# Performance work log

Hardware: AMD Instinct MI355X
Metric: run time of the kernel (lower is better)

The kernel has to match this reference:

```python
import jax, jax.numpy as jnp
import numpy as np

S, B, L = 64, 32, 64
VS, VT = 32000, 32000
D_EMB, H_ENC, H_DEC = 300, 512, 1024


def _lstm_cell(x, h, c, w_ih, w_hh, b):
    # PyTorch gate order: i, f, g, o
    g = x @ w_ih.T + h @ w_hh.T + b
    i, f, gg, o = jnp.split(g, 4, axis=1)
    c2 = jax.nn.sigmoid(f) * c + jax.nn.sigmoid(i) * jnp.tanh(gg)
    h2 = jax.nn.sigmoid(o) * jnp.tanh(c2)
    return h2, c2


def _lstm_dir(emb, w_ih, w_hh, b, reverse):
    h0 = jnp.zeros((emb.shape[1], H_ENC), emb.dtype)
    def step(carry, x):
        h, c = carry
        h, c = _lstm_cell(x, h, c, w_ih, w_hh, b)
        return (h, c), h
    (hT, cT), ys = jax.lax.scan(step, (h0, h0), emb, reverse=reverse)
    return ys, hT, cT


def setup_inputs() -> dict:
    key = jax.random.key(0)
    ks = jax.random.split(key, 20)
    r = lambda k, shape: (jax.random.normal(k, shape, jnp.float32) * 0.02)
    inp = {
        "eemb": r(ks[0], (VS, D_EMB)),
        "enc_w_ih_f": r(ks[1], (4 * H_ENC, D_EMB)),
        "enc_w_hh_f": r(ks[2], (4 * H_ENC, H_ENC)),
        "enc_b_f": r(ks[3], (4 * H_ENC,)),  # = b_ih + b_hh (summed, identical math)
        "enc_w_ih_b": r(ks[4], (4 * H_ENC, D_EMB)),
        "enc_w_hh_b": r(ks[5], (4 * H_ENC, H_ENC)),
        "enc_b_b": r(ks[6], (4 * H_ENC,)),
        "attn_wi": r(ks[7], (H_DEC, H_DEC)),
        "attn_wo": r(ks[8], (H_DEC, 2 * H_DEC)),
        "dec_w_ih": r(ks[9], (4 * H_DEC, H_DEC + D_EMB)),
        "dec_w_hh": r(ks[10], (4 * H_DEC, H_DEC)),
        "dec_b": r(ks[11], (4 * H_DEC,)),
        "demb": r(ks[12], (VT, D_EMB)),
        "gen_w": r(ks[13], (VT, H_DEC)),
        "gen_b": r(ks[14], (VT,)),
        "input_src_batch": jax.random.randint(ks[15], (S, B), 0, VS),
        "input_trg_batch": jax.random.randint(ks[16], (L, B), 0, VT),
    }
    return inp


def reference(eemb, enc_w_ih_f, enc_w_hh_f, enc_b_f, enc_w_ih_b, enc_w_hh_b,
              enc_b_b, attn_wi, attn_wo, dec_w_ih, dec_w_hh, dec_b, demb,
              gen_w, gen_b, input_src_batch, input_trg_batch):
    emb = eemb[input_src_batch]  # [S,B,300]
    out_f, hf, cf = _lstm_dir(emb, enc_w_ih_f, enc_w_hh_f, enc_b_f, False)
    out_b, hb, cb = _lstm_dir(emb, enc_w_ih_b, enc_w_hh_b, enc_b_b, True)
    enc_out = jnp.concatenate([out_f, out_b], axis=2)  # [S,B,1024]
    bsz = emb.shape[1]
    # permute(1,2,0).view(B,1024): interleave fwd/bwd features
    hidden = jnp.stack([hf, hb], 0).transpose(1, 2, 0).reshape(bsz, H_DEC)
    context = jnp.stack([cf, cb], 0).transpose(1, 2, 0).reshape(bsz, H_DEC)

    trg_emb = demb[input_trg_batch[:-1]]  # [L-1,B,300]

    def dec_step(carry, e):
        h, c = carry
        semi = h @ attn_wi.T  # [B,1024]
        scores = jax.nn.softmax(jnp.sum(enc_out * semi[None], axis=2), axis=0)  # [S,B]
        s_tilde = jnp.sum(scores[:, :, None] * enc_out, axis=0)  # [B,1024]
        c_t = jnp.tanh(jnp.concatenate([s_tilde, h], axis=1) @ attn_wo.T)
        x = jnp.concatenate([c_t, e], axis=1)  # [B,1324]
        h, c = _lstm_cell(x, h, c, dec_w_ih, dec_w_hh, dec_b)
        out = jax.nn.log_softmax(h @ gen_w.T + gen_b, axis=1)  # [B,VT]
        return (h, c), out

    _, ys = jax.lax.scan(dec_step, (hidden, context), trg_emb)  # [L-1,B,VT]
    output = jnp.concatenate([jnp.zeros((1,) + ys.shape[1:], ys.dtype), ys], axis=0)
    return output
```

## Files before the change

kernel.cpp:

```cpp
#include <hip/hip_runtime.h>

typedef __attribute__((ext_vector_type(8))) short short8;
typedef __attribute__((ext_vector_type(4))) float f32x4;
typedef unsigned short u16;
typedef unsigned int u32;

static __device__ __forceinline__ float sigf(float x){ return 1.0f/(1.0f+__expf(-x)); }
static __device__ __forceinline__ float ftanh(float x){
    float e = __expf(2.0f*x);
    return 1.0f - 2.0f/(e + 1.0f);
}

static __device__ __forceinline__ u16 f2b(float f){
    u32 u = __float_as_uint(f);
    u += 0x7FFFu + ((u>>16)&1u);
    return (u16)(u>>16);
}
static __device__ __forceinline__ float us2f(u16 s){ return __uint_as_float(((u32)s)<<16); }
static __device__ __forceinline__ float b2f_lo(u32 u){ return __uint_as_float(u<<16); }
static __device__ __forceinline__ float b2f_hi(u32 u){ return __uint_as_float(u & 0xffff0000u); }

static __device__ __forceinline__ void st_wt_u16(u16* p, u16 v) {
    asm volatile("global_store_short %0, %1, off sc1" :: "v"(p), "v"((u32)v) : "memory");
}
static __device__ __forceinline__ void st_wt_u32(u32* p, u32 v) {
    asm volatile("global_store_dword %0, %1, off sc1" :: "v"(p), "v"(v) : "memory");
}
static __device__ __forceinline__ u32 ld_cv(const u32* p){
    u32 v;
    asm volatile("global_load_dword %0, %1, off sc0 sc1\ns_waitcnt vmcnt(0)"
                 : "=v"(v) : "v"(p) : "memory");
    return v;
}

static __device__ __forceinline__ void hot_spin() {
    float x = 1.0f;
#pragma unroll
    for (int i = 0; i < 16; ++i) x = __builtin_fmaf(x, 1.0000001f, 1.0e-7f);
    asm volatile("" :: "v"(x));
}

static __device__ __forceinline__ void wait_publish(const u32* base, int n, u32 tgt, u32* rel) {
    if ((int)threadIdx.x < n) {
        const u32* p = base + (size_t)threadIdx.x*32;
        while (ld_cv(p) < tgt) hot_spin();
    }
    __syncthreads();
    if (threadIdx.x == 0) st_wt_u32(rel, tgt);
}
static __device__ __forceinline__ void wait_rel(const u32* rel, u32 tgt) {
    if (threadIdx.x == 0) {
        while (ld_cv(rel) < tgt) hot_spin();
    }
    __syncthreads();
}


__global__ __launch_bounds__(256) void k_zero(float* __restrict__ p, long n) {
    for (long i = (long)blockIdx.x*256 + threadIdx.x; i < n; i += (long)gridDim.x*256) p[i] = 0.0f;
}

__global__ __launch_bounds__(256) void k_wenc2(const float* __restrict__ whhf,
                                               const float* __restrict__ whhb,
                                               u16* __restrict__ dst) {
    long i = (long)blockIdx.x*256 + threadIdx.x;
    int half = (int)(i >> 20);
    int ii = (int)(i & 1048575);
    int n = ii >> 9, k = ii & 511;
    int j = n >> 2, q = n & 3;
    const float* w = half ? whhb : whhf;
    dst[i] = f2b(w[(size_t)(q*512 + j)*512 + k]);
}

__global__ __launch_bounds__(256) void k_xw(const float* __restrict__ table,
                                            const int* __restrict__ idx,
                                            const float* __restrict__ W,
                                            int wstride, int koff,
                                            const float* __restrict__ bias,
                                            u16* __restrict__ outU, int N,
                                            int jmask, int jshift) {
    __shared__ float Xs[32][300];
    int m0 = blockIdx.y * 32;
    int j0 = blockIdx.x * 64;
    for (int i = threadIdx.x; i < 32*300; i += 256) {
        int r = i/300, c = i - r*300;
        Xs[r][c] = table[(size_t)idx[m0+r]*300 + c];
    }
    __syncthreads();
    int tx = threadIdx.x & 63, ty = threadIdx.x >> 6;
    int jj = j0 + tx;
    const float* wr = W + (size_t)jj*wstride + koff;
    float acc[8] = {0,0,0,0,0,0,0,0};
    for (int k = 0; k < 300; ++k) {
        float w = wr[k];
#pragma unroll
        for (int mi = 0; mi < 8; ++mi) acc[mi] += Xs[ty*8+mi][k] * w;
    }
    float bv = bias[jj];
    int col = ((jj & jmask) << 2) | (jj >> jshift);
#pragma unroll
    for (int mi = 0; mi < 8; ++mi)
        outU[(size_t)(m0 + ty*8 + mi)*N + col] = f2b(acc[mi] + bv);
}

__global__ __launch_bounds__(512, 1) void k_enc(
    const u16* __restrict__ Xf, const u16* __restrict__ Xb,
    const u16* __restrict__ WencB,
    u16* __restrict__ encBX, float* __restrict__ cfin,
    u32* __restrict__ sentE, u32* __restrict__ relE,
    const float* __restrict__ awi, const float* __restrict__ awo,
    const float* __restrict__ dwih, const float* __restrict__ dwhh,
    const float* __restrict__ genw,
    u16* __restrict__ awiTB, u16* __restrict__ awoB,
    u16* __restrict__ WdecB, u16* __restrict__ genw_b)
{
    __shared__ float SH[2304];
    const int tid = threadIdx.x;
    const int bid = blockIdx.x;

    if (bid >= 64) {
        long wid = (long)(bid-64)*512 + tid;
        {
            const float4* s4 = (const float4*)genw;
            ushort4* d4 = (ushort4*)genw_b;
            for (long i = wid; i < 8192000L; i += 98304L) {
                float4 v = s4[i]; ushort4 u;
                u.x=f2b(v.x); u.y=f2b(v.y); u.z=f2b(v.z); u.w=f2b(v.w);
                d4[i]=u;
            }
        }
        for (long i = wid; i < 8388608L; i += 98304L) {
            int n=(int)(i>>11), k=(int)(i&2047);
            int j=n>>2, q=n&3;
            float v=(k<1024)? dwih[(size_t)(q*1024+j)*1324+k]
                            : dwhh[(size_t)(q*1024+j)*1024+(k-1024)];
            WdecB[i]=f2b(v);
        }
        for (long i = wid; i < 1048576L; i += 98304L) {
            int kcol=(int)(i>>10), n=(int)(i&1023);
            awiTB[i]=f2b(awi[(size_t)n*1024+kcol]);
        }
        {
            const float4* s4=(const float4*)awo;
            ushort4* d4=(ushort4*)awoB;
            for (long i = wid; i < 524288L; i += 98304L) {
                float4 v=s4[i]; ushort4 u;
                u.x=f2b(v.x); u.y=f2b(v.y); u.z=f2b(v.z); u.w=f2b(v.w);
                d4[i]=u;
            }
        }
        return;
    }

    const int wv = tid >> 6, lane = tid & 63;
    const int gwave = bid*8 + wv;
    const int lr = lane & 15, lk8 = (lane >> 4)*8;
    const int b_l = lane & 15, jjq = lane >> 4;
    const int g0 = bid & 48;
    u32* relg = relE + (size_t)(g0 >> 4)*32;

    const int dir = gwave >> 8;
    const int mt = (gwave >> 7) & 1;
    const int nt = gwave & 127;
    const int m0 = mt*16, n0 = nt*16;
    const u16* Bw = WencB + (size_t)dir*1048576 + (size_t)(n0+lr)*512 + lk8;
    const u16* Xd = dir ? Xb : Xf;
    float* T = SH + wv*272;
    const int bb = m0 + b_l;
    const int j = nt*4 + jjq;

    short8 bw[16];
#pragma unroll
    for (int i = 0; i < 16; ++i) bw[i] = *(const short8*)(Bw + i*32);

    float creg = 0.f;
    for (int t = 0; t < 64; ++t) {
        if (t > 0) {
            if (bid == g0) wait_publish(sentE + (size_t)g0*32, 16, (u32)t, relg);
            else           wait_rel(relg, (u32)t);
        }
        const int rslot = (t==0) ? 0 : (dir ? (65-t) : t);
        const u16* Ah = encBX + (size_t)rslot*32768 + (size_t)(m0+lr)*1024 + dir*512 + lk8;
        short8 av[16];
#pragma unroll
        for (int i = 0; i < 16; ++i) av[i] = *(const short8*)(Ah + i*32);
        f32x4 acc = {0.f,0.f,0.f,0.f};
#pragma unroll
        for (int i = 0; i < 16; ++i)
            acc = __builtin_amdgcn_mfma_f32_16x16x32_bf16(av[i], bw[i], acc, 0, 0, 0);
        {
            const int rb = (lane>>4)*4;
#pragma unroll
            for (int r = 0; r < 4; ++r) T[(rb+r)*17 + (lane&15)] = acc[r];
        }
        __builtin_amdgcn_sched_barrier(0);
        const int s = dir ? (63-t) : t;
        ushort4 xr = *(const ushort4*)(Xd + (size_t)(s*32+bb)*2048 + n0 + jjq*4);
        float gi = T[b_l*17 + jjq*4 + 0] + us2f(xr.x);
        float gf = T[b_l*17 + jjq*4 + 1] + us2f(xr.y);
        float gg = T[b_l*17 + jjq*4 + 2] + us2f(xr.z);
        float go = T[b_l*17 + jjq*4 + 3] + us2f(xr.w);
        float c2 = sigf(gf)*creg + sigf(gi)*ftanh(gg);
        float h2 = sigf(go)*ftanh(c2);
        creg = c2;
        st_wt_u16(encBX + (size_t)(s+1)*32768 + (size_t)bb*1024 + dir*512 + j, f2b(h2));
        __syncthreads();
        if (tid == 0) st_wt_u32(sentE + (size_t)bid*32, (u32)(t+1));
    }
    cfin[dir*16384 + bb*512 + j] = creg;
}

__global__ __launch_bounds__(256) void k_mid(const u16* __restrict__ encBX,
                                             const u16* __restrict__ awiTB,
                                             const u16* __restrict__ awoB,
                                             u16* __restrict__ encPB,
                                             u16* __restrict__ EOAb,
                                             u16* __restrict__ Hd) {
    if (blockIdx.x < 128) {
        int gt = blockIdx.x*256 + threadIdx.x;
        int b = gt >> 10, jj2 = gt & 1023;
        int d = jj2 & 1, k = jj2 >> 1;
        Hd[(size_t)b*1024 + jj2] = encBX[(size_t)(d ? 1 : 64)*32768 + (size_t)b*1024 + d*512 + k];
        Hd[(size_t)64*32768 + gt] = 0;
    }
    const int wv = threadIdx.x >> 6, lane = threadIdx.x & 63;
    const int lr = lane & 15, lk8 = (lane >> 4)*8;
    const u16* Abase = encBX + 32768;
#pragma unroll
    for (int ii = 0; ii < 4; ++ii) {
        int id = (blockIdx.x*4 + wv)*4 + ii;
        int eoa = id >> 13;
        int id2 = id & 8191;
        int mt2 = id2 >> 6, nt2 = id2 & 63;
        int m0 = mt2*16, n0 = nt2*16;
        const u16* Ar = Abase + (size_t)(m0+lr)*1024 + lk8;
        const u16* Br = eoa ? (awoB + (size_t)(n0+lr)*2048 + lk8)
                            : (awiTB + (size_t)(n0+lr)*1024 + lk8);
        f32x4 acc = {0.f,0.f,0.f,0.f};
#pragma unroll 8
        for (int i = 0; i < 32; ++i) {
            short8 av = *(const short8*)(Ar + i*32);
            short8 bv = *(const short8*)(Br + i*32);
            acc = __builtin_amdgcn_mfma_f32_16x16x32_bf16(av, bv, acc, 0, 0, 0);
        }
        int col = n0 + (lane&15);
        int rb = m0 + (lane>>4)*4;
#pragma unroll
        for (int r = 0; r < 4; ++r) {
            int row = rb + r;
            if (eoa) {
                int b = row & 31, s = row >> 5;
                EOAb[((size_t)b*64 + s)*1024 + col] = f2b(acc[r]);
            } else {
                encPB[(size_t)row*1024 + col] = f2b(acc[r]);
            }
        }
    }
}

__global__ __launch_bounds__(512, 1) void k_dec(
    const u16* __restrict__ Xe,
    const u16* __restrict__ awoB, const u16* __restrict__ WdecB,
    const u16* __restrict__ encPB, const u16* __restrict__ EOAb,
    u16* __restrict__ Hd, u16* __restrict__ PEOb, u16* __restrict__ hAb,
    const float* __restrict__ cfin,
    const u16* __restrict__ genw_b, const float* __restrict__ genb, float* __restrict__ out,
    u32* __restrict__ sentA, u32* __restrict__ sentH,
    u32* __restrict__ relA, u32* __restrict__ relH)
{
    __shared__ float SH[5184];
    __shared__ u32 CT[16512];
    const int tid = threadIdx.x;
    const int bid = blockIdx.x;
    const int wv = tid >> 6, lane = tid & 63;
    const int lr = lane & 15, lk8 = (lane >> 4)*8;
    const int b_l = lane & 15, jjq = lane >> 4;

    if (bid >= 128) {
        const int gw = (bid - 128)*8 + wv;
        const u16* A = Hd + 32768;
        for (int c = 0; c < 8; ++c) {
            u32 need = (c == 7) ? 63u : (u32)(8*c + 8);
            wait_rel(relH, need);
            int tile = gw;
            if (tile < 1000) {
                int m0 = c*256 + (tile & 1)*128;
                int n0 = (tile >> 1)*64;
                f32x4 acc[8][4] = {};
                for (int k0 = 0; k0 < 1024; k0 += 32) {
                    short8 bfr[4];
#pragma unroll
                    for (int ni = 0; ni < 4; ++ni)
                        bfr[ni] = *(const short8*)(genw_b + (size_t)(n0 + ni*16 + lr)*1024 + k0 + lk8);
#pragma unroll
                    for (int mi = 0; mi < 8; ++mi) {
                        short8 a = *(const short8*)(A + (size_t)(m0 + mi*16 + lr)*1024 + k0 + lk8);
#pragma unroll
                        for (int ni = 0; ni < 4; ++ni)
                            acc[mi][ni] = __builtin_amdgcn_mfma_f32_16x16x32_bf16(a, bfr[ni], acc[mi][ni], 0, 0, 0);
                    }
                }
                int dcol = lane & 15;
                int drow = (lane >> 4)*4;
#pragma unroll
                for (int mi = 0; mi < 8; ++mi) {
                    int mbase = m0 + mi*16 + drow;
#pragma unroll
                    for (int ni = 0; ni < 4; ++ni) {
                        int n = n0 + ni*16 + dcol;
                        float bv = genb[n];
                        f32x4 v = acc[mi][ni];
#pragma unroll
                        for (int r = 0; r < 4; ++r) {
                            int m = mbase + r;
                            if (m < 2016) out[(size_t)(m + 32)*32000 + n] = v[r] + bv;
                        }
                    }
                }
            }
        }
        return;
    }

    const int ntB = wv & 1, kqB = wv >> 1;
    const int jdB = bid*8 + ntB*4 + jjq;
    float cdec0 = 0.f, cdec1 = 0.f;
    if (wv < 2) {
        cdec0 = cfin[(jdB&1)*16384 + (b_l)*512 + (jdB>>1)];
        cdec1 = cfin[(jdB&1)*16384 + (16+b_l)*512 + (jdB>>1)];
    }

    short8 wp[16];
#pragma unroll
    for (int i = 0; i < 16; ++i)
        wp[i] = *(const short8*)(WdecB + (size_t)(bid*32 + ntB*16 + lr)*2048 + kqB*512 + lk8 + i*32);

    const bool isHA = (bid >= 32 && bid < 96);
    const int nth = bid - 32;
    const int mth = wv & 1, kqh = wv >> 1;
    short8 wh[8];
    if (isHA) {
#pragma unroll
        for (int i = 0; i < 8; ++i)
            wh[i] = *(const short8*)(awoB + (size_t)(nth*16+lr)*2048 + 1024 + kqh*256 + lk8 + i*32);
    }

    for (int t = 0; t < 63; ++t) {
        if (t > 0 && bid == 97) wait_publish(sentH, 128, (u32)t, relH);
        if (bid < 96) {
            if (t > 0) wait_rel(relH, (u32)t);
            if (bid < 32) {
                const int b = bid;
                float* hsh = SH; float* red = SH + 1024; float* sc = SH + 1536;
                {
                    u32 u = ((const u32*)Hd)[(size_t)t*16384 + b*512 + tid];
                    hsh[2*tid]   = b2f_lo(u);
                    hsh[2*tid+1] = b2f_hi(u);
                }
                __syncthreads();
                {
                    int s = tid >> 3, p = tid & 7;
                    const uint4* ep = (const uint4*)(encPB + (size_t)(s*32+b)*1024 + p*128);
                    const float* hk = hsh + p*128;
                    float a0=0,a1=0,a2=0,a3=0;
#pragma unroll 4
                    for (int q8 = 0; q8 < 16; ++q8) {
                        uint4 u = ep[q8];
                        a0 += b2f_lo(u.x)*hk[q8*8+0] + b2f_hi(u.x)*hk[q8*8+1];
                        a1 += b2f_lo(u.y)*hk[q8*8+2] + b2f_hi(u.y)*hk[q8*8+3];
                        a2 += b2f_lo(u.z)*hk[q8*8+4] + b2f_hi(u.z)*hk[q8*8+5];
                        a3 += b2f_lo(u.w)*hk[q8*8+6] + b2f_hi(u.w)*hk[q8*8+7];
                    }
                    red[tid] = (a0+a1)+(a2+a3);
                }
                __syncthreads();
                if (tid < 64) {
                    float v = 0;
#pragma unroll
                    for (int pp = 0; pp < 8; ++pp) v += red[tid*8+pp];
                    float m = v;
                    for (int off = 32; off; off >>= 1) m = fmaxf(m, __shfl_xor(m, off));
                    float e = __expf(v - m);
                    float ss = e;
                    for (int off = 32; off; off >>= 1) ss += __shfl_xor(ss, off);
                    sc[tid] = e / ss;
                }
                __syncthreads();
                {
                    const u32* eo = (const u32*)EOAb + (size_t)b*32768 + tid;
                    float p0 = 0, p1 = 0;
#pragma unroll 8
                    for (int s = 0; s < 64; ++s) {
                        u32 u = eo[(size_t)s*512];
                        float w = sc[s];
                        p0 += w*b2f_lo(u); p1 += w*b2f_hi(u);
                    }
                    u32 pk = (u32)f2b(p0) | ((u32)f2b(p1) << 16);
                    st_wt_u32((u32*)PEOb + (size_t)t*16384 + b*512 + tid, pk);
                }
            } else {
                const u16* Ah = Hd + (size_t)t*32768 + (size_t)(mth*16+lr)*1024 + kqh*256 + lk8;
                short8 av[8];
#pragma unroll
                for (int i = 0; i < 8; ++i) av[i] = *(const short8*)(Ah + i*32);
                f32x4 acc = {0.f,0.f,0.f,0.f};
#pragma unroll
                for (int i = 0; i < 8; ++i)
                    acc = __builtin_amdgcn_mfma_f32_16x16x32_bf16(av[i], wh[i], acc, 0, 0, 0);
#pragma unroll
                for (int r = 0; r < 4; ++r) SH[wv*256 + lane*4 + r] = acc[r];
                __syncthreads();
                if (wv < 2) {
#pragma unroll
                    for (int r = 0; r < 4; ++r) {
                        float sum = SH[(wv+0)*256 + lane*4 + r] + SH[(wv+2)*256 + lane*4 + r]
                                  + SH[(wv+4)*256 + lane*4 + r] + SH[(wv+6)*256 + lane*4 + r];
                        int m = wv*16 + (lane>>4)*4 + r;
                        st_wt_u16(hAb + (size_t)t*32768 + (size_t)m*1024 + nth*16 + (lane&15),
                                  f2b(sum));
                    }
                }
            }
            __syncthreads();
            if (tid == 0) st_wt_u32(sentA + (size_t)bid*32, (u32)(t+1));
        }

        if (bid == 96) wait_publish(sentA, 96, (u32)(t+1), relA);
        else           wait_rel(relA, (u32)(t+1));
        {
            const u32* pe = (const u32*)PEOb + (size_t)t*16384;
            const u32* ha = (const u32*)hAb + (size_t)t*16384;
#pragma unroll
            for (int ii = 0; ii < 32; ++ii) {
                int idx = tid + ii*512;
                u32 up = pe[idx], uh = ha[idx];
                float c0 = ftanh(b2f_lo(up) + b2f_lo(uh));
                float c1 = ftanh(b2f_hi(up) + b2f_hi(uh));
                int b = idx >> 9, nu = idx & 511;
                CT[b*516 + nu] = (u32)f2b(c0) | ((u32)f2b(c1) << 16);
            }
            __syncthreads();

            f32x4 a0 = {0.f,0.f,0.f,0.f}, a1 = {0.f,0.f,0.f,0.f};
            if (kqB < 2) {
                const u32* c0p = CT + (lr)*516 + kqB*256 + (lk8 >> 1);
                const u32* c1p = CT + (16+lr)*516 + kqB*256 + (lk8 >> 1);
#pragma unroll
                for (int i = 0; i < 16; ++i) {
                    short8 v0 = *(const short8*)(c0p + i*16);
                    short8 v1 = *(const short8*)(c1p + i*16);
                    a0 = __builtin_amdgcn_mfma_f32_16x16x32_bf16(v0, wp[i], a0, 0, 0, 0);
                    a1 = __builtin_amdgcn_mfma_f32_16x16x32_bf16(v1, wp[i], a1, 0, 0, 0);
                }
            } else {
                const u16* h0p = Hd + (size_t)t*32768 + (size_t)(lr)*1024 + (kqB-2)*512 + lk8;
                const u16* h1p = Hd + (size_t)t*32768 + (size_t)(16+lr)*1024 + (kqB-2)*512 + lk8;
#pragma unroll
                for (int i = 0; i < 16; ++i) {
                    short8 v0 = *(const short8*)(h0p + i*32);
                    short8 v1 = *(const short8*)(h1p + i*32);
                    a0 = __builtin_amdgcn_mfma_f32_16x16x32_bf16(v0, wp[i], a0, 0, 0, 0);
                    a1 = __builtin_amdgcn_mfma_f32_16x16x32_bf16(v1, wp[i], a1, 0, 0, 0);
                }
            }
#pragma unroll
            for (int r = 0; r < 4; ++r) {
                SH[wv*512 + lane*4 + r] = a0[r];
                SH[wv*512 + 256 + lane*4 + r] = a1[r];
            }
            __syncthreads();
            if (wv < 2) {
                const int nt = wv;
                float* T0 = SH + 4096 + (wv*2+0)*272;
                float* T1 = SH + 4096 + (wv*2+1)*272;
#pragma unroll
                for (int r = 0; r < 4; ++r) {
                    float s0 = SH[(nt+0)*512 + lane*4 + r] + SH[(nt+2)*512 + lane*4 + r]
                             + SH[(nt+4)*512 + lane*4 + r] + SH[(nt+6)*512 + lane*4 + r];
                    float s1 = SH[(nt+0)*512 + 256 + lane*4 + r] + SH[(nt+2)*512 + 256 + lane*4 + r]
                             + SH[(nt+4)*512 + 256 + lane*4 + r] + SH[(nt+6)*512 + 256 + lane*4 + r];
                    int rr = ((lane>>4)*4 + r)*17 + (lane&15);
                    T0[rr] = s0;
                    T1[rr] = s1;
                }
                __builtin_amdgcn_sched_barrier(0);
                {
                    ushort4 xr = *(const ushort4*)(Xe + (size_t)(t*32 + b_l)*4096 + jdB*4);
                    float gi = T0[b_l*17 + jjq*4 + 0] + us2f(xr.x);
                    float gf = T0[b_l*17 + jjq*4 + 1] + us2f(xr.y);
                    float gg = T0[b_l*17 + jjq*4 + 2] + us2f(xr.z);
                    float go = T0[b_l*17 + jjq*4 + 3] + us2f(xr.w);
                    float c2 = sigf(gf)*cdec0 + sigf(gi)*ftanh(gg);
                    float h2 = sigf(go)*ftanh(c2);
                    cdec0 = c2;
                    st_wt_u16(Hd + (size_t)(t+1)*32768 + (size_t)b_l*1024 + jdB, f2b(h2));
                }
                {
                    ushort4 xr = *(const ushort4*)(Xe + (size_t)(t*32 + 16 + b_l)*4096 + jdB*4);
                    float gi = T1[b_l*17 + jjq*4 + 0] + us2f(xr.x);
                    float gf = T1[b_l*17 + jjq*4 + 1] + us2f(xr.y);
                    float gg = T1[b_l*17 + jjq*4 + 2] + us2f(xr.z);
                    float go = T1[b_l*17 + jjq*4 + 3] + us2f(xr.w);
                    float c2 = sigf(gf)*cdec1 + sigf(gi)*ftanh(gg);
                    float h2 = sigf(go)*ftanh(c2);
                    cdec1 = c2;
                    st_wt_u16(Hd + (size_t)(t+1)*32768 + (size_t)(16+b_l)*1024 + jdB, f2b(h2));
                }
            }
            __syncthreads();
            if (tid == 0) st_wt_u32(sentH + (size_t)bid*32, (u32)(t+1));
        }
    }
    if (bid == 97) wait_publish(sentH, 128, 63u, relH);
}

__global__ __launch_bounds__(256) void k_lsm(float* __restrict__ out) {
    long row = 32 + blockIdx.x;
    float* p = out + row*32000L;
    float4* p4 = (float4*)p;
    int tid = threadIdx.x;
    __shared__ float sm[4];
    __shared__ float ss[4];
    float m = -1e30f;
    for (int i = tid; i < 8000; i += 256) {
        float4 v = p4[i];
        m = fmaxf(m, fmaxf(fmaxf(v.x, v.y), fmaxf(v.z, v.w)));
    }
    for (int off = 32; off; off >>= 1) m = fmaxf(m, __shfl_xor(m, off));
    if ((tid & 63) == 0) sm[tid >> 6] = m;
    __syncthreads();
    m = fmaxf(fmaxf(sm[0], sm[1]), fmaxf(sm[2], sm[3]));
    float s = 0;
    for (int i = tid; i < 8000; i += 256) {
        float4 v = p4[i];
        s += __expf(v.x - m) + __expf(v.y - m) + __expf(v.z - m) + __expf(v.w - m);
    }
    for (int off = 32; off; off >>= 1) s += __shfl_xor(s, off);
    if ((tid & 63) == 0) ss[tid >> 6] = s;
    __syncthreads();
    s = ss[0] + ss[1] + ss[2] + ss[3];
    float lse = m + __logf(s);
    for (int i = tid; i < 8000; i += 256) {
        float4 v = p4[i];
        v.x -= lse; v.y -= lse; v.z -= lse; v.w -= lse;
        p4[i] = v;
    }
}


extern "C" void kernel_launch(void* const* d_in, const int* in_sizes, int n_in,
                              void* d_out, int out_size, void* d_ws, size_t ws_size,
                              hipStream_t stream) {
    const float* eemb  = (const float*)d_in[0];
    const float* ewihf = (const float*)d_in[1];
    const float* ewhhf = (const float*)d_in[2];
    const float* ebf   = (const float*)d_in[3];
    const float* ewihb = (const float*)d_in[4];
    const float* ewhhb = (const float*)d_in[5];
    const float* ebb   = (const float*)d_in[6];
    const float* awi   = (const float*)d_in[7];
    const float* awo   = (const float*)d_in[8];
    const float* dwih  = (const float*)d_in[9];
    const float* dwhh  = (const float*)d_in[10];
    const float* db    = (const float*)d_in[11];
    const float* demb  = (const float*)d_in[12];
    const float* genw  = (const float*)d_in[13];
    const float* genb  = (const float*)d_in[14];
    const int* srci    = (const int*)d_in[15];
    const int* trgi    = (const int*)d_in[16];
    float* out = (float*)d_out;

    float* F = (float*)d_ws;
    u32* S       = (u32*)F;
    u32* sentE   = S;
    u32* sentA   = S + 2048;
    u32* sentH   = S + 5120;
    u32* relE    = S + 13312;
    u32* relA    = S + 13440;
    u32* relH    = S + 13472;
    float* cfin  = F + 16384;
    u16*   U     = (u16*)(F + 49152);

    u16* Xf_    = U;
    u16* Xb_    = U + 4194304u;
    u16* Xe_    = U + 8388608u;
    u16* WencB  = U + 16646144u;
    u16* awiTB  = U + 18743296u;
    u16* awoB   = U + 19791872u;
    u16* WdecB  = U + 21889024u;
    u16* genw_b = U + 30277632u;
    u16* encBX  = U + 63045632u;
    u16* Hd     = U + 65175552u;
    u16* PEOb   = U + 67305472u;
    u16* hAb    = U + 69369856u;
    u16* encPB  = U + 71434240u;
    u16* EOAb   = U + 73531392u;

    k_zero<<<64, 256, 0, stream>>>(F, 16384);
    k_zero<<<64, 256, 0, stream>>>((float*)encBX, 16384);
    k_zero<<<2048, 256, 0, stream>>>(out, 1024000L);

    k_xw<<<dim3(32, 64), 256, 0, stream>>>(eemb, srci, ewihf, 300, 0, ebf, Xf_, 2048, 511, 9);
    k_xw<<<dim3(32, 64), 256, 0, stream>>>(eemb, srci, ewihb, 300, 0, ebb, Xb_, 2048, 511, 9);
    k_xw<<<dim3(64, 63), 256, 0, stream>>>(demb, trgi, dwih, 1324, 1024, db, Xe_, 4096, 1023, 10);

    k_wenc2<<<8192, 256, 0, stream>>>(ewhhf, ewhhb, WencB);

    k_enc<<<256, 512, 0, stream>>>(Xf_, Xb_, WencB, encBX, cfin, sentE, relE,
                                   awi, awo, dwih, dwhh, genw,
                                   awiTB, awoB, WdecB, genw_b);
    k_mid<<<1024, 256, 0, stream>>>(encBX, awiTB, awoB, encPB, EOAb, Hd);

    k_dec<<<256, 512, 0, stream>>>(Xe_, awoB, WdecB, encPB, EOAb,
                                   Hd, PEOb, hAb, cfin,
                                   genw_b, genb, out,
                                   sentA, sentH, relA, relH);

    k_lsm<<<2016, 256, 0, stream>>>(out);
}
```

Measured before the change: 2.480 ms.

## Halve encoder LSTM blocks with two N-tiles per wave and fold zeroing into weight prep

The encoder recurrence now uses 32 blocks instead of 64, with each wave computing two 16-column tiles that share one A-operand load per step. Each synchronisation group shrinks from 16 to 8 blocks, which cuts barrier fan-in per timestep. The freed blocks are handed to the weight-conversion work, so 224 blocks now do it. The two separate zeroing launches are folded into the weight-prep kernel. The cost is twice the MFMA work and register pressure per wave on the serial critical path.

Result: slower. 2.570 ms (+3.6%).

```diff
diff --git a/kernel.cpp b/kernel.cpp
--- a/kernel.cpp
+++ b/kernel.cpp
@@ -62,7 +62,14 @@
 
 __global__ __launch_bounds__(256) void k_wenc2(const float* __restrict__ whhf,
                                                const float* __restrict__ whhb,
-                                               u16* __restrict__ dst) {
+                                               u16* __restrict__ dst,
+                                               float* __restrict__ sentF,
+                                               float* __restrict__ encBX0) {
+    if (blockIdx.x < 64) {
+        sentF[blockIdx.x*256 + threadIdx.x] = 0.0f;
+    } else if (blockIdx.x < 128) {
+        encBX0[(blockIdx.x-64)*256 + threadIdx.x] = 0.0f;
+    }
     long i = (long)blockIdx.x*256 + threadIdx.x;
     int half = (int)(i >> 20);
     int ii = (int)(i & 1048575);
@@ -114,36 +121,36 @@
     u16* __restrict__ awiTB, u16* __restrict__ awoB,
     u16* __restrict__ WdecB, u16* __restrict__ genw_b)
 {
-    __shared__ float SH[2304];
+    __shared__ float SH[4224];
     const int tid = threadIdx.x;
     const int bid = blockIdx.x;
 
-    if (bid >= 64) {
-        long wid = (long)(bid-64)*512 + tid;
+    if (bid >= 32) {
+        long wid = (long)(bid-32)*512 + tid;
         {
             const float4* s4 = (const float4*)genw;
             ushort4* d4 = (ushort4*)genw_b;
-            for (long i = wid; i < 8192000L; i += 98304L) {
+            for (long i = wid; i < 8192000L; i += 114688L) {
                 float4 v = s4[i]; ushort4 u;
                 u.x=f2b(v.x); u.y=f2b(v.y); u.z=f2b(v.z); u.w=f2b(v.w);
                 d4[i]=u;
             }
         }
-        for (long i = wid; i < 8388608L; i += 98304L) {
+        for (long i = wid; i < 8388608L; i += 114688L) {
             int n=(int)(i>>11), k=(int)(i&2047);
             int j=n>>2, q=n&3;
             float v=(k<1024)? dwih[(size_t)(q*1024+j)*1324+k]
                             : dwhh[(size_t)(q*1024+j)*1024+(k-1024)];
             WdecB[i]=f2b(v);
         }
-        for (long i = wid; i < 1048576L; i += 98304L) {
+        for (long i = wid; i < 1048576L; i += 114688L) {
             int kcol=(int)(i>>10), n=(int)(i&1023);
             awiTB[i]=f2b(awi[(size_t)n*1024+kcol]);
         }
         {
             const float4* s4=(const float4*)awo;
             ushort4* d4=(ushort4*)awoB;
-            for (long i = wid; i < 524288L; i += 98304L) {
+            for (long i = wid; i < 524288L; i += 114688L) {
                 float4 v=s4[i]; ushort4 u;
                 u.x=f2b(v.x); u.y=f2b(v.y); u.z=f2b(v.z); u.w=f2b(v.w);
                 d4[i]=u;
@@ -153,61 +160,74 @@
     }
 
     const int wv = tid >> 6, lane = tid & 63;
-    const int gwave = bid*8 + wv;
     const int lr = lane & 15, lk8 = (lane >> 4)*8;
     const int b_l = lane & 15, jjq = lane >> 4;
-    const int g0 = bid & 48;
-    u32* relg = relE + (size_t)(g0 >> 4)*32;
-
-    const int dir = gwave >> 8;
-    const int mt = (gwave >> 7) & 1;
-    const int nt = gwave & 127;
-    const int m0 = mt*16, n0 = nt*16;
-    const u16* Bw = WencB + (size_t)dir*1048576 + (size_t)(n0+lr)*512 + lk8;
+
+    const int dir = bid >> 4;
+    const int mt  = (bid >> 3) & 1;
+    const int g0  = bid & 24;
+    u32* relg = relE + (size_t)(g0 >> 3)*32;
+
+    const int n0 = ((bid & 7)*8 + wv)*32;
+    const int m0 = mt*16;
     const u16* Xd = dir ? Xb : Xf;
-    float* T = SH + wv*272;
+    float* T = SH + wv*528;
     const int bb = m0 + b_l;
-    const int j = nt*4 + jjq;
-
-    short8 bw[16];
-#pragma unroll
-    for (int i = 0; i < 16; ++i) bw[i] = *(const short8*)(Bw + i*32);
-
-    float creg = 0.f;
+    const int jb = n0 >> 2;
+
+    short8 bw0[16], bw1[16];
+    {
+        const u16* B0 = WencB + (size_t)dir*1048576 + (size_t)(n0+lr)*512 + lk8;
+        const u16* B1 = WencB + (size_t)dir*1048576 + (size_t)(n0+16+lr)*512 + lk8;
+#pragma unroll
+        for (int i = 0; i < 16; ++i) { bw0[i] = *(const short8*)(B0 + i*32);
+                                       bw1[i] = *(const short8*)(B1 + i*32); }
+    }
+
+    float creg[2] = {0.f, 0.f};
     for (int t = 0; t < 64; ++t) {
         if (t > 0) {
-            if (bid == g0) wait_publish(sentE + (size_t)g0*32, 16, (u32)t, relg);
+            if (bid == g0) wait_publish(sentE + (size_t)g0*32, 8, (u32)t, relg);
             else           wait_rel(relg, (u32)t);
         }
         const int rslot = (t==0) ? 0 : (dir ? (65-t) : t);
         const u16* Ah = encBX + (size_t)rslot*32768 + (size_t)(m0+lr)*1024 + dir*512 + lk8;
-        short8 av[16];
-#pragma unroll
-        for (int i = 0; i < 16; ++i) av[i] = *(const short8*)(Ah + i*32);
-        f32x4 acc = {0.f,0.f,0.f,0.f};
-#pragma unroll
-        for (int i = 0; i < 16; ++i)
-            acc = __builtin_amdgcn_mfma_f32_16x16x32_bf16(av[i], bw[i], acc, 0, 0, 0);
+        f32x4 acc0 = {0.f,0.f,0.f,0.f}, acc1 = {0.f,0.f,0.f,0.f};
+#pragma unroll
+        for (int i = 0; i < 16; ++i) {
+            short8 av = *(const short8*)(Ah + i*32);
+            acc0 = __builtin_amdgcn_mfma_f32_16x16x32_bf16(av, bw0[i], acc0, 0, 0, 0);
+            acc1 = __builtin_amdgcn_mfma_f32_16x16x32_bf16(av, bw1[i], acc1, 0, 0, 0);
+        }
         {
             const int rb = (lane>>4)*4;
 #pragma unroll
-            for (int r = 0; r < 4; ++r) T[(rb+r)*17 + (lane&15)] = acc[r];
+            for (int r = 0; r < 4; ++r) {
+                T[(rb+r)*33 + (lane&15)]      = acc0[r];
+                T[(rb+r)*33 + 16 + (lane&15)] = acc1[r];
+            }
         }
         __builtin_amdgcn_sched_barrier(0);
         const int s = dir ? (63-t) : t;
-        ushort4 xr = *(const ushort4*)(Xd + (size_t)(s*32+bb)*2048 + n0 + jjq*4);
-        float gi = T[b_l*17 + jjq*4 + 0] + us2f(xr.x);
-        float gf = T[b_l*17 + jjq*4 + 1] + us2f(xr.y);
-        float gg = T[b_l*17 + jjq*4 + 2] + us2f(xr.z);
-        float go = T[b_l*17 + jjq*4 + 3] + us2f(xr.w);
-        float c2 = sigf(gf)*creg + sigf(gi)*ftanh(gg);
-        float h2 = sigf(go)*ftanh(c2);
-        creg = c2;
-        st_wt_u16(encBX + (size_t)(s+1)*32768 + (size_t)bb*1024 + dir*512 + j, f2b(h2));
+#pragma unroll
+        for (int jj2 = 0; jj2 < 2; ++jj2) {
+            const int j = jb + jj2*4 + jjq;
+            ushort4 xr = *(const ushort4*)(Xd + (size_t)(s*32+bb)*2048 + j*4);
+            float gi = T[b_l*33 + jj2*16 + jjq*4 + 0] + us2f(xr.x);
+            float gf = T[b_l*33 + jj2*16 + jjq*4 + 1] + us2f(xr.y);
+            float gg = T[b_l*33 + jj2*16 + jjq*4 + 2] + us2f(xr.z);
+            float go = T[b_l*33 + jj2*16 + jjq*4 + 3] + us2f(xr.w);
+            float c2 = sigf(gf)*creg[jj2] + sigf(gi)*ftanh(gg);
+            float h2 = sigf(go)*ftanh(c2);
+            creg[jj2] = c2;
+            st_wt_u16(encBX + (size_t)(s+1)*32768 + (size_t)bb*1024 + dir*512 + j, f2b(h2));
+        }
         __syncthreads();
         if (tid == 0) st_wt_u32(sentE + (size_t)bid*32, (u32)(t+1));
     }
-    cfin[dir*16384 + bb*512 + j] = creg;
+#pragma unroll
+    for (int jj2 = 0; jj2 < 2; ++jj2)
+        cfin[dir*16384 + bb*512 + (jb + jj2*4 + jjq)] = creg[jj2];
 }
 
 __global__ __launch_bounds__(256) void k_mid(const u16* __restrict__ encBX,
@@ -596,15 +616,13 @@
     u16* encPB  = U + 71434240u;
     u16* EOAb   = U + 73531392u;
 
-    k_zero<<<64, 256, 0, stream>>>(F, 16384);
-    k_zero<<<64, 256, 0, stream>>>((float*)encBX, 16384);
     k_zero<<<2048, 256, 0, stream>>>(out, 1024000L);
 
     k_xw<<<dim3(32, 64), 256, 0, stream>>>(eemb, srci, ewihf, 300, 0, ebf, Xf_, 2048, 511, 9);
     k_xw<<<dim3(32, 64), 256, 0, stream>>>(eemb, srci, ewihb, 300, 0, ebb, Xb_, 2048, 511, 9);
     k_xw<<<dim3(64, 63), 256, 0, stream>>>(demb, trgi, dwih, 1324, 1024, db, Xe_, 4096, 1023, 10);
 
-    k_wenc2<<<8192, 256, 0, stream>>>(ewhhf, ewhhb, WencB);
+    k_wenc2<<<8192, 256, 0, stream>>>(ewhhf, ewhhb, WencB, F, (float*)encBX);
 
     k_enc<<<256, 512, 0, stream>>>(Xf_, Xb_, WencB, encBX, cfin, sentE, relE,
                                    awi, awo, dwih, dwhh, genw,
```
